# Kernel tuning notes

Hardware: AMD Instinct MI355X
Metric: run time of the kernel (lower is better)

The kernel has to match this reference:

```python
import jax, jax.numpy as jnp
import numpy as np

BIT = 128
Y_P = 0.5
RIGHT = BIT / 8.0
LEFT = RIGHT / 2.0
UB = BIT / 2.0
ALPHA = 0.1
PCT_NUM, PCT_DEN = 9, 10  # percent = 9/10
C_COEF = (1.0 / RIGHT) * np.log(Y_P / (99.0 * (1.0 - Y_P)))  # slope c (constant since y_p fixed)
A_COEF = -1.0 / (LEFT * C_COEF) * np.log(99.0 * Y_P / (1.0 - Y_P))  # hard-branch factor a
# with y_p=0.5: d = -c*BP, g = -a*c*BP, so f_easy = c*(x-BP), f_hard = a*c*(x-BP)


def setup_inputs() -> dict:
    key = jax.random.key(0)
    k1, k2 = jax.random.split(key)
    N, C = 6144, 200
    u = jax.random.normal(k1, (N, BIT), dtype=jnp.float32)
    labels = jax.random.randint(k2, (N,), 0, C)
    y = jax.nn.one_hot(labels, C, dtype=jnp.int32)
    ind = jnp.arange(N, dtype=jnp.int32)  # unused dataset indices
    return {"u": u, "y": y, "ind": ind}


def reference(u, y, ind):
    sg = jax.lax.stop_gradient
    N = u.shape[0]
    uh = jnp.tanh(u)
    s = (y @ y.T) > 0                      # [N,N] bool similarity (diagonal is True)
    inner = uh @ uh.T                      # [N,N]
    n_sim = s.sum(axis=1)                  # int per-row similar count
    n_dis = N - n_sim
    fn_sim = n_sim.astype(jnp.float32)
    fn_dis = n_dis.astype(jnp.float32)
    idx = jnp.arange(N)[None, :]

    meanS = jnp.clip(jnp.where(s, inner, 0.0).sum(1) / jnp.maximum(fn_sim, 1.0), 0.0, UB)
    meanDS = jnp.clip(jnp.where(s, 0.0, inner).sum(1) / jnp.maximum(fn_dis, 1.0), 0.0, UB)

    dis_sorted = jnp.sort(jnp.where(s, -jnp.inf, inner), axis=1)
    start_dis = (n_dis * PCT_NUM) // PCT_DEN          # int(len*0.9)
    tail_mask = idx >= (N - n_dis + start_dis)[:, None]
    tail_cnt = jnp.maximum((n_dis - start_dis).astype(jnp.float32), 1.0)
    dMax = jnp.clip(jnp.where(tail_mask, dis_sorted, 0.0).sum(1) / tail_cnt, 0.0, UB)

    sim_sorted = jnp.sort(jnp.where(s, inner, jnp.inf), axis=1)
    start_sim = (n_sim * PCT_NUM) // PCT_DEN
    head_mask = idx < (n_sim - start_sim)[:, None]
    head_cnt = jnp.maximum((n_sim - start_sim).astype(jnp.float32), 1.0)
    sMin = jnp.clip(jnp.where(head_mask, sim_sorted, 0.0).sum(1) / head_cnt, 0.0, UB)

    # .item() in the original detaches these -> stop_gradient
    meanS, meanDS, dMax, sMin = map(sg, (meanS, meanDS, dMax, sMin))
    BP = meanS - (UB - meanS) / UB * jnp.abs(meanS - dMax)      # [N]
    BPd = meanDS + meanDS / UB * jnp.abs(meanDS - sMin)         # [N]

    # similar-pair loss: f + log(1+exp(-f)) == softplus(f)
    dc = inner - BP[:, None]
    f_sim = jnp.where(inner > BP[:, None], C_COEF * dc, A_COEF * C_COEF * dc)
    mask_sim = s & (inner != BP[:, None])             # == BP excluded in torch indexing
    cnt_sim = jnp.maximum(mask_sim.sum(1).astype(jnp.float32), 1.0)
    row_pos = jnp.where(mask_sim, jax.nn.softplus(f_sim), 0.0).sum(1) / cnt_sim

    # dissimilar-pair loss: log(1+exp(-f)) == softplus(-f)
    dcd = inner - BPd[:, None]
    f_dis = jnp.where(inner < BPd[:, None], C_COEF * dcd, A_COEF * C_COEF * dcd)
    mask_dis = (~s) & (inner != BPd[:, None])
    cnt_dis = jnp.maximum(mask_dis.sum(1).astype(jnp.float32), 1.0)
    row_neg = jnp.where(mask_dis, jax.nn.softplus(-f_dis), 0.0).sum(1) / cnt_dis

    valid = (n_sim > 0) & (n_dis > 0)
    count = valid.sum().astype(jnp.float32)
    posL = jnp.where(count > 0, jnp.where(valid, row_pos, 0.0).sum() / jnp.maximum(count, 1.0), 0.0)
    navL = jnp.where(count > 0, jnp.where(valid, row_neg, 0.0).sum() / jnp.maximum(count, 1.0), 0.0)

    q_loss = ALPHA * jnp.mean((uh - jnp.sign(uh)) ** 2)
    return posL + navL + q_loss
```

## Files before the change

### kernel.cpp

```cpp
#include <hip/hip_runtime.h>
#include <cstdint>

#define NROW 6144
#define KDIM 128
#define NLAB 200
#define C_COEF (-0.28719499063341177f)
#define UBV 64.0f

typedef _Float16 f16x8 __attribute__((ext_vector_type(8)));
typedef _Float16 f16x2 __attribute__((ext_vector_type(2)));
typedef float f32x4 __attribute__((ext_vector_type(4)));
typedef __attribute__((address_space(1))) const void as1c_void;
typedef __attribute__((address_space(3))) void as3_void;

union U8 { f16x8 h; unsigned u[4]; f16x2 p[4]; };
union CV16 { _Float16 h; unsigned short us; };

__device__ __forceinline__ float softplus_f(float x){
  return fmaxf(x, 0.f) + __logf(1.f + __expf(-fabsf(x)));
}
__device__ __forceinline__ float waveRedF(float v){
#pragma unroll
  for (int o = 32; o; o >>= 1) v += __shfl_down(v, o, 64);
  return v;
}
__device__ __forceinline__ float bfRedF(float v){
#pragma unroll
  for (int o = 32; o; o >>= 1) v += __shfl_xor(v, o, 64);
  return v;
}
__device__ __forceinline__ int bfRedI(int v){
#pragma unroll
  for (int o = 32; o; o >>= 1) v += __shfl_xor(v, o, 64);
  return v;
}
__device__ __forceinline__ int bfMaxI(int v){
#pragma unroll
  for (int o = 32; o; o >>= 1){ int x = __shfl_xor(v, o, 64); v = v > x ? v : x; }
  return v;
}
__device__ __forceinline__ float bfMaxF(float v){
#pragma unroll
  for (int o = 32; o; o >>= 1) v = fmaxf(v, __shfl_xor(v, o, 64));
  return v;
}
__device__ __forceinline__ float val_of_key(unsigned key){
  unsigned bits = (key & 0x8000u) ? (key ^ 0x8000u) : (key ^ 0xFFFFu);
  CV16 cv; cv.us = (unsigned short)bits;
  return (float)cv.h;
}

__global__ __launch_bounds__(256) void k_labtanh(const int* __restrict__ y,
    unsigned char* __restrict__ lab, int* __restrict__ cnt, int* __restrict__ simIdx,
    const float* __restrict__ u, _Float16* __restrict__ uhswz, float* __restrict__ accf){
  const int bid = blockIdx.x;
  const int tid = threadIdx.x;
  if (bid < NROW){
    if (tid < NLAB && y[(size_t)bid * NLAB + tid] != 0){
      lab[bid] = (unsigned char)tid;
      int p = atomicAdd(&cnt[tid], 1);
      if (p < 512) simIdx[tid * 512 + p] = bid;
    }
    return;
  }
  const int gid = (bid - NROW) * 256 + tid;
  const int row = gid >> 4;
  const int h = gid & 15;
  const int g = h ^ (row & 7);
  const float* sp = u + (size_t)row * KDIM + g * 8;
  float q = 0.f;
  f16x8 o;
#pragma unroll
  for (int t = 0; t < 8; t++){
    float x = sp[t];
    float e2 = __expf(2.f * x);
    float th = 1.f - 2.f * __builtin_amdgcn_rcpf(e2 + 1.f);
    float sg = (th > 0.f) ? 1.f : ((th < 0.f) ? -1.f : 0.f);
    float d = th - sg;
    q += d * d;
    o[t] = (_Float16)th;
  }
  *(f16x8*)(uhswz + (size_t)row * KDIM + h * 8) = o;
  q = waveRedF(q);
  __shared__ float qb[4];
  if ((tid & 63) == 0) qb[tid >> 6] = q;
  __syncthreads();
  if (tid == 0) atomicAdd(&accf[0], qb[0] + qb[1] + qb[2] + qb[3]);
}

__global__ __launch_bounds__(256) void k_mm(const _Float16* __restrict__ A,
    _Float16* __restrict__ out, int row0){
  __shared__ __align__(16) _Float16 SH[2 * 128 * KDIM];
  _Float16* As = SH;
  _Float16* Bs = SH + 128 * KDIM;
  const int tid = threadIdx.x;
  const int wav = tid >> 6, lane = tid & 63;
  const int bj = blockIdx.x, bi = blockIdx.y;

  const char* Ag = (const char*)(A + (size_t)(row0 + bi * 128) * KDIM);
  const char* Bg = (const char*)(A + (size_t)(bj * 128) * KDIM);
  char* Asb = (char*)As;
  char* Bsb = (char*)Bs;
#pragma unroll
  for (int t = 0; t < 8; t++){
    const int ub = wav * 8192 + t * 1024;
    __builtin_amdgcn_global_load_lds((as1c_void*)(Ag + ub + lane * 16),
                                     (as3_void*)(Asb + ub), 16, 0, 0);
    __builtin_amdgcn_global_load_lds((as1c_void*)(Bg + ub + lane * 16),
                                     (as3_void*)(Bsb + ub), 16, 0, 0);
  }
  __syncthreads();

  const int quad = lane >> 4, l16 = lane & 15;
  const int wm = (wav >> 1) * 64, wn = (wav & 1) * 64;
  f32x4 acc[4][4];
#pragma unroll
  for (int im = 0; im < 4; im++)
#pragma unroll
    for (int in = 0; in < 4; in++)
      acc[im][in] = (f32x4){0.f, 0.f, 0.f, 0.f};

#pragma unroll
  for (int kb = 0; kb < 4; kb++){
    f16x8 af[4], bf[4];
#pragma unroll
    for (int i = 0; i < 4; i++){
      const int m = wm + i * 16 + l16;
      const int gidx = kb * 4 + quad;
      af[i] = *(const f16x8*)(Asb + m * 256 + ((gidx ^ (m & 7)) << 4));
      const int n = wn + i * 16 + l16;
      bf[i] = *(const f16x8*)(Bsb + n * 256 + ((gidx ^ (n & 7)) << 4));
    }
#pragma unroll
    for (int im = 0; im < 4; im++)
#pragma unroll
      for (int in = 0; in < 4; in++)
        acc[im][in] = __builtin_amdgcn_mfma_f32_16x16x32_f16(af[im], bf[in], acc[im][in], 0, 0, 0);
  }
  __syncthreads();

  _Float16* Cs = SH;
#pragma unroll
  for (int im = 0; im < 4; im++)
#pragma unroll
    for (int in = 0; in < 4; in++)
#pragma unroll
      for (int r = 0; r < 4; r++){
        const int rl = wm + im * 16 + quad * 4 + r;
        const int cl = wn + in * 16 + l16;
        Cs[rl * 132 + cl] = (_Float16)acc[im][in][r];
      }
  __syncthreads();

  _Float16* obase = out + (size_t)(bi * 128) * NROW + (size_t)bj * 128;
  const int s = tid & 15;
#pragma unroll
  for (int i = 0; i < 8; i++){
    const int r = (tid >> 4) + i * 16;
    f16x8 vv = *(const f16x8*)(Cs + r * 132 + s * 8);
    *(f16x8*)(obase + (size_t)r * NROW + s * 8) = vv;
  }
}

__global__ __launch_bounds__(256) void k_stats(const _Float16* __restrict__ buf,
    const unsigned char* __restrict__ lab, const int* __restrict__ cnt,
    const int* __restrict__ simIdx, float* __restrict__ rowRes, int row0){
  __shared__ int   histS[4][1028];
  __shared__ float simvS[4][512];
  const int tid = threadIdx.x;
  const int lane = tid & 63;
  const int wav = tid >> 6;
  const int lrow = blockIdx.x * 4 + wav;
  const int row = row0 + lrow;
  const int myl = lab[row];
  const int n_sim = cnt[myl];
  const int n_dis = NROW - n_sim;
  if (n_dis == 0 || n_sim == 0) return;
  const int k1 = n_dis - (n_dis * 9) / 10;
  const int k2 = n_sim - (n_sim * 9) / 10;
  const int ns = (n_sim < 512) ? n_sim : 512;

  int*   hist = histS[wav];
  int*   myh  = hist + (lane >> 4) * 257;
  float* simv = simvS[wav];
#pragma unroll
  for (int r = 0; r < 4; r++) *(int4*)&hist[(lane + 64 * r) * 4] = make_int4(0, 0, 0, 0);
  if (lane == 0) *(int4*)&hist[1024] = make_int4(0, 0, 0, 0);

  const f16x8* src = (const f16x8*)(buf + (size_t)lrow * NROW);
  const _Float16* srcs = buf + (size_t)lrow * NROW;

  float sumAll = 0.f;
  const f16x2 ones = (f16x2){(_Float16)1.f, (_Float16)1.f};
#pragma unroll 1
  for (int it = 0; it < 12; ++it){
    U8 x; x.h = src[it * 64 + lane];
#pragma unroll
    for (int k = 0; k < 4; k++){
      unsigned wv = x.u[k];
      unsigned m = (wv >> 15) & 0x00010001u;
      unsigned key2 = wv ^ 0x80008000u ^ (m * 0x7FFFu);
      atomicAdd(&myh[(key2 >> 8) & 0xFFu], 1);
      atomicAdd(&myh[key2 >> 24], 1);
#if __has_builtin(__builtin_amdgcn_fdot2)
      sumAll = __builtin_amdgcn_fdot2(x.p[k], ones, sumAll, false);
#else
      sumAll += (float)x.h[2 * k] + (float)x.h[2 * k + 1];
#endif
    }
  }

  float sumS = 0.f;
  for (int t = lane; t < ns; t += 64){
    int idx = simIdx[myl * 512 + t];
    CV16 cv; cv.h = srcs[idx];
    unsigned bits = (unsigned)cv.us;
    unsigned key = bits ^ 0x8000u ^ ((bits >> 15) * 0x7FFFu);
    float v = (float)cv.h;
    simv[t] = v; sumS += v;
    atomicAdd(&myh[key >> 8], -1);
  }
  sumAll = bfRedF(sumAll);
  sumS = bfRedF(sumS);
  const float sumD = sumAll - sumS;

  int cArr[4];
#pragma unroll
  for (int d = 0; d < 4; d++){
    const int b = 4 * lane + d;
    cArr[d] = hist[b] + hist[257 + b] + hist[514 + b] + hist[771 + b];
  }
  int part = cArr[0] + cArr[1] + cArr[2] + cArr[3];
  int suf = part;
#pragma unroll
  for (int o = 1; o < 64; o <<= 1){
    int x = __shfl_down(suf, o, 64);
    if (lane + o < 64) suf += x;
  }
  int cum = suf - part;
  int encB = -1, krF = 0;
#pragma unroll
  for (int d = 3; d >= 0; --d){
    int cd = cArr[d];
    if (k1 > cum && k1 <= cum + cd){ encB = 4 * lane + d; krF = k1 - cum; }
    cum += cd;
  }
  const int hbStar = bfMaxI(encB);
  const int kr1 = bfMaxI(krF);

#pragma unroll
  for (int r = 0; r < 4; r++) *(int4*)&hist[(lane + 64 * r) * 4] = make_int4(0, 0, 0, 0);
  if (lane == 0) *(int4*)&hist[1024] = make_int4(0, 0, 0, 0);

  float sAb = 0.f;
#pragma unroll 1
  for (int it = 0; it < 12; ++it){
    U8 x; x.h = src[it * 64 + lane];
#pragma unroll
    for (int k = 0; k < 4; k++){
      unsigned wv = x.u[k];
      unsigned m = (wv >> 15) & 0x00010001u;
      unsigned key2 = wv ^ 0x80008000u ^ (m * 0x7FFFu);
      int hbLo = (key2 >> 8) & 0xFF;
      int hbHi = key2 >> 24;
      if (hbLo > hbStar) sAb += (float)x.h[2 * k];
      else if (hbLo == hbStar) atomicAdd(&myh[key2 & 0xFFu], 1);
      if (hbHi > hbStar) sAb += (float)x.h[2 * k + 1];
      else if (hbHi == hbStar) atomicAdd(&myh[(key2 >> 16) & 0xFFu], 1);
    }
  }
  for (int t = lane; t < ns; t += 64){
    float v = simv[t];
    CV16 cv; cv.h = (_Float16)v;
    unsigned bits = (unsigned)cv.us;
    unsigned key = bits ^ 0x8000u ^ ((bits >> 15) * 0x7FFFu);
    int hb = (int)(key >> 8);
    if (hb > hbStar) sAb -= v;
    else if (hb == hbStar) atomicAdd(&myh[key & 0xFFu], -1);
  }
  sAb = bfRedF(sAb);

  int c2[4];
#pragma unroll
  for (int d = 0; d < 4; d++){
    const int b = 4 * lane + d;
    c2[d] = hist[b] + hist[257 + b] + hist[514 + b] + hist[771 + b];
  }
  part = c2[0] + c2[1] + c2[2] + c2[3];
  suf = part;
#pragma unroll
  for (int o = 1; o < 64; o <<= 1){
    int x = __shfl_down(suf, o, 64);
    if (lane + o < 64) suf += x;
  }
  cum = suf - part;
  int encL = -1, g2F = 0;
#pragma unroll
  for (int d = 3; d >= 0; --d){
    int cd = c2[d];
    if (kr1 > cum && kr1 <= cum + cd){ encL = 4 * lane + d; g2F = cum; }
    cum += cd;
  }
  const int lbStar = bfMaxI(encL);
  const int gt2 = bfMaxI(g2F);
  float sumIn = 0.f;
#pragma unroll
  for (int d = 0; d < 4; d++){
    int lb = 4 * lane + d;
    if (lb > lbStar) sumIn += (float)c2[d] * val_of_key((unsigned)((hbStar << 8) | lb));
  }
  sumIn = bfRedF(sumIn);
  const float piv = val_of_key((unsigned)((hbStar << 8) | lbStar));
  const float dSum = sAb + sumIn + (float)(kr1 - gt2) * piv;

  float fpiv2 = -3e38f; int flt = 0;
  for (int t = lane; t < ns; t += 64){
    float vt = simv[t];
    int lt = 0, eq = 0;
    for (int j = 0; j < ns; j++){
      float vj = simv[j];
      lt += (vj < vt); eq += (vj == vt);
    }
    if (lt < k2 && k2 <= lt + eq){ fpiv2 = vt; flt = lt; }
  }
  const float piv2 = bfMaxF(fpiv2);
  const int ltS = bfMaxI(flt);
  float slt = 0.f;
  for (int t = lane; t < ns; t += 64){
    float v = simv[t];
    if (v < piv2) slt += v;
  }
  slt = bfRedF(slt);
  const float sSum = slt + (float)(k2 - ltS) * piv2;

  const float meanS  = fminf(fmaxf(sumS / fmaxf((float)n_sim, 1.f), 0.f), UBV);
  const float meanDS = fminf(fmaxf(sumD / fmaxf((float)n_dis, 1.f), 0.f), UBV);
  const float dMax   = fminf(fmaxf(dSum / fmaxf((float)k1, 1.f), 0.f), UBV);
  const float sMin   = fminf(fmaxf(sSum / fmaxf((float)k2, 1.f), 0.f), UBV);
  const float BP  = meanS - (UBV - meanS) / UBV * fabsf(meanS - dMax);
  const float BPd = meanDS + meanDS / UBV * fabsf(meanDS - sMin);

  float an = 0.f; int ties = 0;
#pragma unroll 1
  for (int it = 0; it < 12; ++it){
    f16x8 h8 = src[it * 64 + lane];
#pragma unroll
    for (int e = 0; e < 8; e++){
      float v = (float)h8[e];
      float dcd = v - BPd;
      float f = ((dcd < 0.f) ? C_COEF : 2.f * C_COEF) * dcd;
      an += softplus_f(-f);
      ties += (dcd == 0.f);
    }
  }
  float spSim = 0.f; int tiesSim = 0;
  float ap = 0.f, cp = 0.f;
  for (int t = lane; t < ns; t += 64){
    float v = simv[t];
    float dcd = v - BPd;
    if (dcd == 0.f) tiesSim++;
    else {
      float f = ((dcd < 0.f) ? C_COEF : 2.f * C_COEF) * dcd;
      spSim += softplus_f(-f);
    }
    if (v != BP){
      float dc = v - BP;
      float f = (v > BP) ? C_COEF * dc : (2.f * C_COEF) * dc;
      ap += softplus_f(f); cp += 1.f;
    }
  }
  an = bfRedF(an); spSim = bfRedF(spSim);
  const int tiesT = bfRedI(ties);
  const int tiesSimT = bfRedI(tiesSim);
  ap = bfRedF(ap); cp = bfRedF(cp);
  if (lane == 0){
    const float L = __logf(1.f + __expf(-0.f));
    float anF = an - (float)tiesT * L - spSim;
    float cnF = (float)(n_dis - (tiesT - tiesSimT));
    float4 r;
    r.x = ap / fmaxf(cp, 1.f);
    r.y = anF / fmaxf(cnF, 1.f);
    r.z = 1.f;
    r.w = 0.f;
    *(float4*)(rowRes + 4 * (size_t)row) = r;
  }
}

__global__ __launch_bounds__(256) void k_final(const float* __restrict__ accf,
    const float* __restrict__ rowRes, float* __restrict__ out){
  const int tid = threadIdx.x;
  float p = 0.f, n = 0.f, c = 0.f;
  for (int i = tid; i < NROW; i += 256){
    float4 r = *(const float4*)(rowRes + 4 * (size_t)i);
    p += r.x; n += r.y; c += r.z;
  }
  p = bfRedF(p); n = bfRedF(n); c = bfRedF(c);
  __shared__ float sb[12];
  const int wav = tid >> 6;
  if ((tid & 63) == 0){ sb[wav] = p; sb[4 + wav] = n; sb[8 + wav] = c; }
  __syncthreads();
  if (tid == 0){
    p = sb[0] + sb[1] + sb[2] + sb[3];
    n = sb[4] + sb[5] + sb[6] + sb[7];
    c = sb[8] + sb[9] + sb[10] + sb[11];
    float posL = 0.f, navL = 0.f;
    if (c > 0.f){ posL = p / c; navL = n / c; }
    out[0] = posL + navL + 0.1f * (accf[0] / (float)(NROW * KDIM));
  }
}

extern "C" void kernel_launch(void* const* d_in, const int* in_sizes, int n_in,
                              void* d_out, int out_size, void* d_ws, size_t ws_size,
                              hipStream_t stream){
  const float* u = (const float*)d_in[0];
  const int* y = (const int*)d_in[1];
  char* ws = (char*)d_ws;
  float* accf = (float*)ws;
  int* cnt = (int*)(ws + 64);
  float* rowRes = (float*)(ws + 4096);
  unsigned char* lab = (unsigned char*)(ws + 102400);
  int* simIdx = (int*)(ws + 108544);
  _Float16* uhswz = (_Float16*)(ws + 518144);
  const size_t ibufOff = 518144 + (size_t)NROW * KDIM * 2;
  _Float16* ibuf = (_Float16*)(ws + ibufOff);

  hipMemsetAsync(d_ws, 0, 102400, stream);
  k_labtanh<<<NROW + (NROW * 16) / 256, 256, 0, stream>>>(y, lab, cnt, simIdx,
                                                          u, uhswz, accf);

  size_t avail = (ws_size > ibufOff) ? ws_size - ibufOff : 0;
  long maxRows = (long)(avail / ((size_t)NROW * 2));
  maxRows = (maxRows / 128) * 128;
  if (maxRows > NROW) maxRows = NROW;
  if (maxRows < 128) maxRows = 128;

  for (int r0 = 0; r0 < NROW; r0 += (int)maxRows){
    int rows = NROW - r0;
    if (rows > maxRows) rows = (int)maxRows;
    k_mm<<<dim3(48, rows / 128), 256, 0, stream>>>(uhswz, ibuf, r0);
    k_stats<<<rows / 4, 256, 0, stream>>>(ibuf, lab, cnt, simIdx, rowRes, r0);
  }
  k_final<<<1, 256, 0, stream>>>(accf, rowRes, (float*)d_out);
}
```

Measured before the change: 170.8 us.

## Exploit Gram symmetry in matmul, vectorize label scan, unroll stats loops

When the full Gram matrix fits in the workspace, the matmul kernel computes only upper-triangle tiles and writes each off-diagonal tile twice, once transposed through shared memory. This roughly halves the MFMA and input-load work, while output writes stay the same and an extra LDS transpose pass is added. The label kernel now reads each one-hot row as int4 with four rows per block, cutting the block count for that phase. The three streaming loops in the stats kernel go from unroll 1 to unroll 2 to expose more memory-level parallelism.

```diff
diff --git a/kernel.cpp b/kernel.cpp
--- a/kernel.cpp
+++ b/kernel.cpp
@@ -55,15 +55,26 @@
     const float* __restrict__ u, _Float16* __restrict__ uhswz, float* __restrict__ accf){
   const int bid = blockIdx.x;
   const int tid = threadIdx.x;
-  if (bid < NROW){
-    if (tid < NLAB && y[(size_t)bid * NLAB + tid] != 0){
-      lab[bid] = (unsigned char)tid;
-      int p = atomicAdd(&cnt[tid], 1);
-      if (p < 512) simIdx[tid * 512 + p] = bid;
+  const int NLB = NROW / 4;
+  if (bid < NLB){
+    const int lane = tid & 63;
+    const int row = bid * 4 + (tid >> 6);
+    if (lane < NLAB / 4){
+      const int4 v = ((const int4*)(y + (size_t)row * NLAB))[lane];
+      int t = -1;
+      if (v.x != 0) t = 4 * lane;
+      if (v.y != 0) t = 4 * lane + 1;
+      if (v.z != 0) t = 4 * lane + 2;
+      if (v.w != 0) t = 4 * lane + 3;
+      if (t >= 0){
+        lab[row] = (unsigned char)t;
+        int p = atomicAdd(&cnt[t], 1);
+        if (p < 512) simIdx[t * 512 + p] = row;
+      }
     }
     return;
   }
-  const int gid = (bid - NROW) * 256 + tid;
+  const int gid = (bid - NLB) * 256 + tid;
   const int row = gid >> 4;
   const int h = gid & 15;
   const int g = h ^ (row & 7);
@@ -89,13 +100,14 @@
 }
 
 __global__ __launch_bounds__(256) void k_mm(const _Float16* __restrict__ A,
-    _Float16* __restrict__ out, int row0){
+    _Float16* __restrict__ out, int row0, int sym){
+  const int bj = blockIdx.x, bi = blockIdx.y;
+  if (sym && bi > bj) return;
   __shared__ __align__(16) _Float16 SH[2 * 128 * KDIM];
   _Float16* As = SH;
   _Float16* Bs = SH + 128 * KDIM;
   const int tid = threadIdx.x;
   const int wav = tid >> 6, lane = tid & 63;
-  const int bj = blockIdx.x, bi = blockIdx.y;
 
   const char* Ag = (const char*)(A + (size_t)(row0 + bi * 128) * KDIM);
   const char* Bg = (const char*)(A + (size_t)(bj * 128) * KDIM);
@@ -159,6 +171,28 @@
     const int r = (tid >> 4) + i * 16;
     f16x8 vv = *(const f16x8*)(Cs + r * 132 + s * 8);
     *(f16x8*)(obase + (size_t)r * NROW + s * 8) = vv;
+  }
+
+  if (sym && bi != bj){
+    __syncthreads();
+#pragma unroll
+    for (int im = 0; im < 4; im++)
+#pragma unroll
+      for (int in = 0; in < 4; in++)
+#pragma unroll
+        for (int r = 0; r < 4; r++){
+          const int rl = wm + im * 16 + quad * 4 + r;
+          const int cl = wn + in * 16 + l16;
+          Cs[cl * 132 + rl] = (_Float16)acc[im][in][r];
+        }
+    __syncthreads();
+    _Float16* obase2 = out + (size_t)(bj * 128) * NROW + (size_t)bi * 128;
+#pragma unroll
+    for (int i = 0; i < 8; i++){
+      const int r = (tid >> 4) + i * 16;
+      f16x8 vv = *(const f16x8*)(Cs + r * 132 + s * 8);
+      *(f16x8*)(obase2 + (size_t)r * NROW + s * 8) = vv;
+    }
   }
 }
 
@@ -192,7 +226,7 @@
 
   float sumAll = 0.f;
   const f16x2 ones = (f16x2){(_Float16)1.f, (_Float16)1.f};
-#pragma unroll 1
+#pragma unroll 2
   for (int it = 0; it < 12; ++it){
     U8 x; x.h = src[it * 64 + lane];
 #pragma unroll
@@ -253,7 +287,7 @@
   if (lane == 0) *(int4*)&hist[1024] = make_int4(0, 0, 0, 0);
 
   float sAb = 0.f;
-#pragma unroll 1
+#pragma unroll 2
   for (int it = 0; it < 12; ++it){
     U8 x; x.h = src[it * 64 + lane];
 #pragma unroll
@@ -341,7 +375,7 @@
   const float BPd = meanDS + meanDS / UBV * fabsf(meanDS - sMin);
 
   float an = 0.f; int ties = 0;
-#pragma unroll 1
+#pragma unroll 2
   for (int it = 0; it < 12; ++it){
     f16x8 h8 = src[it * 64 + lane];
 #pragma unroll
@@ -425,8 +459,8 @@
   _Float16* ibuf = (_Float16*)(ws + ibufOff);
 
   hipMemsetAsync(d_ws, 0, 102400, stream);
-  k_labtanh<<<NROW + (NROW * 16) / 256, 256, 0, stream>>>(y, lab, cnt, simIdx,
-                                                          u, uhswz, accf);
+  k_labtanh<<<NROW / 4 + (NROW * 16) / 256, 256, 0, stream>>>(y, lab, cnt, simIdx,
+                                                              u, uhswz, accf);
 
   size_t avail = (ws_size > ibufOff) ? ws_size - ibufOff : 0;
   long maxRows = (long)(avail / ((size_t)NROW * 2));
@@ -437,7 +471,8 @@
   for (int r0 = 0; r0 < NROW; r0 += (int)maxRows){
     int rows = NROW - r0;
     if (rows > maxRows) rows = (int)maxRows;
-    k_mm<<<dim3(48, rows / 128), 256, 0, stream>>>(uhswz, ibuf, r0);
+    const int sym = (rows == NROW) ? 1 : 0;
+    k_mm<<<dim3(48, rows / 128), 256, 0, stream>>>(uhswz, ibuf, r0, sym);
     k_stats<<<rows / 4, 256, 0, stream>>>(ibuf, lab, cnt, simIdx, rowRes, r0);
   }
   k_final<<<1, 256, 0, stream>>>(accf, rowRes, (float*)d_out);
```

Result: no change. 168.6 us (-1.3%).
